# Kernel optimization log

Measured on AMD Instinct MI355X. Metric: run time of the kernel, lower is better.

## Reference

```python
import jax, jax.numpy as jnp
import numpy as np

B, T, D = 2, 2048, 2048
NH, NKV = 16, 4
HD = D // NH  # 128
BASE, TSL = 10000.0, 1024


def rotary_tables(T, hd, base=BASE, tsl=TSL):
    # Matches Rotary.forward with rd == hd (rd=0 in __init__ -> full head dim).
    ar = jnp.arange(0, hd, 2, dtype=jnp.float32) / hd
    if T <= tsl:
        inv = 1.0 / (base ** ar)
    else:
        # NTK-style rescale; note right-assoc exponent in original torch code:
        # 1/(base * (T/tsl) ** ((rd/(rd-2)) ** ar))
        inv = 1.0 / (base * jnp.power(T / tsl, jnp.power(hd / (hd - 2.0), ar)))
    f = jnp.outer(jnp.arange(T, dtype=jnp.float32), inv)  # [T, hd//2]
    cos = jnp.cos(f)[None, :, None, :]  # [1,T,1,hd//2]
    sin = jnp.sin(f)[None, :, None, :]
    return cos, sin


def apply_rope(x, cos, sin):
    # full-dim rope: split halves, rotate
    h = x.shape[-1] // 2
    x1, x2 = x[..., :h], x[..., h:]
    return jnp.concatenate((x1 * cos + x2 * sin, -x1 * sin + x2 * cos), axis=-1)


def rms_norm(x):
    eps = jnp.finfo(x.dtype).eps
    return x * jax.lax.rsqrt(jnp.mean(x * x, axis=-1, keepdims=True) + eps)


def setup_inputs() -> dict:
    key = jax.random.key(0)
    k0, k1, k2, k3, k4 = jax.random.split(key, 5)
    s = 0.02
    return {
        "x": jax.random.normal(k0, (B, T, D), jnp.float32),
        "qw": jax.random.normal(k1, (NH * HD, D), jnp.float32) * s,
        "kw": jax.random.normal(k2, (NKV * HD, D), jnp.float32) * s,
        "vw": jax.random.normal(k3, (NKV * HD, D), jnp.float32) * s,
        "ow": jax.random.normal(k4, (D, D), jnp.float32) * s,
        "qg": jnp.ones((NH,), jnp.float32),
    }


def reference(x, qw, kw, vw, ow, qg):
    Bx, Tx, Dx = x.shape
    q = (x @ qw.T).reshape(Bx, Tx, NH, HD)
    k = (x @ kw.T).reshape(Bx, Tx, NKV, HD)
    v = (x @ vw.T).reshape(Bx, Tx, NKV, HD)
    q = rms_norm(q)
    k = rms_norm(k)
    cos, sin = rotary_tables(Tx, HD)
    q = apply_rope(q, cos, sin) * qg[None, None, :, None]
    k = apply_rope(k, cos, sin)
    # GQA: repeat kv heads
    r = NH // NKV
    k = jnp.repeat(k, r, axis=2)  # [B,T,NH,HD]
    v = jnp.repeat(v, r, axis=2)
    scale = 1.0 / jnp.sqrt(jnp.asarray(HD, q.dtype))
    scores = jnp.einsum("bqhd,bkhd->bhqk", q, k) * scale  # [B,NH,T,T]
    causal = jnp.tril(jnp.ones((Tx, Tx), dtype=bool))
    scores = jnp.where(causal[None, None, :, :], scores, jnp.asarray(-jnp.inf, scores.dtype))
    attn = jax.nn.softmax(scores, axis=-1)
    y = jnp.einsum("bhqk,bkhd->bqhd", attn, v)  # [B,T,NH,HD]
    return y.reshape(Bx, Tx, Dx) @ ow.T
```

## Files before the change

### kernel.cpp

```cpp
#include <hip/hip_runtime.h>
#include <hip/hip_bf16.h>
#include <stdint.h>


typedef __attribute__((ext_vector_type(8))) short short8;
typedef __attribute__((ext_vector_type(4))) float f32x4;
typedef __attribute__((ext_vector_type(16))) float f32x16;

#define GLOAD16(gp, lp) \
  __builtin_amdgcn_global_load_lds((const __attribute__((address_space(1))) void*)(gp), \
                                   (__attribute__((address_space(3))) void*)(lp), 16, 0, 0)

#define BAR() do { asm volatile("" ::: "memory"); __builtin_amdgcn_s_barrier(); asm volatile("" ::: "memory"); } while (0)

__device__ __forceinline__ float bf2f(unsigned short u) {
  union { unsigned int i; float f; } v; v.i = ((unsigned int)u) << 16; return v.f;
}
__device__ __forceinline__ unsigned short f2bf(float f) {
  union { float fl; unsigned int i; } v; v.fl = f;
  unsigned int r = v.i + 0x7fffu + ((v.i >> 16) & 1u);
  return (unsigned short)(r >> 16);
}
__device__ __forceinline__ unsigned pk2(float a, float b) {
  return (unsigned)f2bf(a) | ((unsigned)f2bf(b) << 16);
// ... 151 lines not shown
#pragma unroll
      for (int ks = 0; ks < 2; ++ks) af[iq][ks] = *(const short8*)(Ab + oA[iq][ks]);
#pragma unroll
    for (int jj = 0; jj < JQ; ++jj)
#pragma unroll
      for (int ks = 0; ks < 2; ++ks) b0[jj][ks] = *(const short8*)(Bb + oB[jj][ks]);
    MM(0, 0, b0);
    BAR();
    if (s + 2 < NS) STA((s + 2) << 6, 0, dq);
#pragma unroll
    for (int jj = 0; jj < JQ; ++jj)
#pragma unroll
      for (int ks = 0; ks < 2; ++ks) b1[jj][ks] = *(const short8*)(Bb + BSZ + oB[jj][ks]);
    MM(0, 1, b1);
    BAR();
    if (s + 2 < NS) STB((s + 2) << 6, 0, dq);
#pragma unroll
    for (int iq = 0; iq < IQ; ++iq)
#pragma unroll
      for (int ks = 0; ks < 2; ++ks) af[iq][ks] = *(const short8*)(Ab + ASZ + oA[iq][ks]);
    MM(1, 0, b0);
    BAR();
    if (s + 2 < NS) STB((s + 2) << 6, 1, dq);
    MM(1, 1, b1);
    if (s + 2 < NS) VMC(); else VM0();
    BAR();
  }
#undef VMC
#undef VM0
#undef MM

#pragma unroll
  for (int ih = 0; ih < 2; ++ih)
#pragma unroll
    for (int iq = 0; iq < IQ; ++iq) {
      int row = m0 + wr * 2 * S + ih * S + iq * 16 + lane_g * 4;
#pragma unroll
      for (int jh = 0; jh < 2; ++jh)
#pragma unroll
        for (int jj = 0; jj < JQ; ++jj) {
          int col = n0 + wc * (NB / 4) + jh * (NB / 8) + jj * 16 + lane_r;
#pragma unroll
          for (int r = 0; r < 4; ++r) {
            float v = acc[ih * IQ + iq][jh * JQ + jj][r];
            if (OUTF)
              ((float*)Cp)[(size_t)(row + r) * N + col] = v;
            else
              ((unsigned short*)Cp)[(size_t)(row + r) * N + col] = f2bf(v);
          }
        }
    }
}

__global__ __launch_bounds__(256) void normrope_kernel(unsigned short* __restrict__ qkv,
                                                       const float* __restrict__ cost,
                                                       const float* __restrict__ sint,
                                                       const float* __restrict__ qg) {
  const int tid = threadIdx.x, l = tid & 63, w = tid >> 6;
  int row = blockIdx.x * 4 + w;
  int tok = row / 20, hh = row - tok * 20;
  int t = tok & 2047;
  bool isq = hh < 16;
  int col0 = isq ? hh * 128 : 2048 + (hh - 16) * 128;
  unsigned short* p = qkv + (size_t)tok * 3072 + col0 + 2 * l;
  unsigned int u = *(const unsigned int*)p;
  float x0 = bf2f((unsigned short)(u & 0xffffu));
  float x1 = bf2f((unsigned short)(u >> 16));
  float ss = x0 * x0 + x1 * x1;
#pragma unroll
  for (int m = 1; m < 64; m <<= 1) ss += __shfl_xor(ss, m);
  float rn = rsqrtf(ss * (1.0f / 128.0f) + 1.1920928955078125e-07f);
  float n0 = x0 * rn, n1 = x1 * rn;
  float p0 = __shfl_xor(n0, 32);
  float p1 = __shfl_xor(n1, 32);
  int jj = (2 * l) & 63;
  float c0 = cost[t * 64 + jj], c1 = cost[t * 64 + jj + 1];
  float s0 = sint[t * 64 + jj], s1 = sint[t * 64 + jj + 1];
  float o0, o1;
  if (l < 32) { o0 = n0 * c0 + p0 * s0; o1 = n1 * c1 + p1 * s1; }
  else        { o0 = -p0 * s0 + n0 * c0; o1 = -p1 * s1 + n1 * c1; }
  if (isq) { float g = qg[hh] * 0.08838834764831845f * 1.4426950408889634f; o0 *= g; o1 *= g; }
  *(unsigned int*)p = pk2(o0, o1);
}

__global__ __launch_bounds__(256) void vtrans_kernel(const unsigned short* __restrict__ qkv,
                                                     unsigned short* __restrict__ vtg) {
  __shared__ unsigned short tile[64][132];
  int bid = blockIdx.x;
  int pan = bid & 7, tt = bid >> 3;
  int b = pan >> 2, kvh = pan & 3;
  int t0 = tt * 64;
  const unsigned short* src = qkv + ((size_t)(b * 2048 + t0)) * 3072 + 2560 + kvh * 128;
#pragma unroll
  for (int i = 0; i < 8; ++i) {
    int idx = i * 256 + threadIdx.x;
    int row = idx >> 5, c4 = idx & 31;
    uint2 v = *(const uint2*)(src + (size_t)row * 3072 + c4 * 4);
    *(uint2*)&tile[row][c4 * 4] = v;
  }
  __syncthreads();
  unsigned short* dst = vtg + (size_t)pan * 262144 + t0;
#pragma unroll
  for (int i = 0; i < 8; ++i) {
    int idx = i * 256 + threadIdx.x;
    int d = idx >> 4, tc = idx & 15;
    unsigned short a0 = tile[tc * 4 + 0][d], a1 = tile[tc * 4 + 1][d];
    unsigned short a2 = tile[tc * 4 + 2][d], a3 = tile[tc * 4 + 3][d];
    uint2 o; o.x = (unsigned)a0 | ((unsigned)a1 << 16);
    o.y = (unsigned)a2 | ((unsigned)a3 << 16);
    *(uint2*)(dst + (size_t)d * 2048 + tc * 4) = o;
  }
}

__global__ __launch_bounds__(512) void attn_fa7(const unsigned short* __restrict__ qkv,
                                                const unsigned short* __restrict__ vtg,
                                                unsigned short* __restrict__ y) {
  extern __shared__ char smc[];
  const int tid = threadIdx.x;
  const int l = tid & 63, w = tid >> 6;
  const int lq = l & 31, hi = l >> 5;
  const int g = w & 3, hh = w >> 2;

  int n = blockIdx.x;
  int pan = n & 7;
  int b = pan >> 2, kvh = pan & 3;
  int idx2 = n >> 3;
  int h = kvh * 4 + (idx2 & 3);
  int pairIdx = idx2 >> 2;
  const size_t rowbase = (size_t)b * 2048;
  const unsigned short* kvK = qkv + rowbase * 3072;
  const unsigned short* vtp = vtg + (size_t)pan * 262144;

  int kg[2], vg[2], sl[2];
#pragma unroll
  for (int t = 0; t < 2; ++t) {
    int idx = t * 512 + tid;
    { int row = idx >> 4, c = idx & 15, gc = c ^ (row & 7);
      kg[t] = row * 3072 + 2048 + kvh * 128 + gc * 8; }
    { int d = idx >> 3, c = idx & 7, gc = c ^ (d & 7);
      vg[t] = d * 2048 + gc * 8; }
    sl[t] = idx * 16;
  }
  const int swq = (lq & 7) << 4;
  const int krow = (hh * 32 + lq) * 256;
  int oxk[8];
#pragma unroll
  for (int ds = 0; ds < 8; ++ds) oxk[ds] = (ds * 32 + hi * 16) ^ swq;
  const int vrow = lq * 128;
  int oxv[2];
#pragma unroll
  for (int ksl = 0; ksl < 2; ++ksl) oxv[ksl] = (hh * 64 + ksl * 32 + hi * 16) ^ swq;
  const int mab = (g * 64 + l) * 256;
  const int mlb = 65536 + (g * 64 + l) * 8;
  const int lsw = (l & 7) << 4;

  auto STAGE = [&](int tile, int bufsel) {
    const unsigned short* srcK = kvK + (size_t)tile * 64 * 3072;
    const unsigned short* srcV = vtp + tile * 64;
    char* kd = smc + bufsel * 16384;
    char* vd = smc + 32768 + bufsel * 16384;
#pragma unroll
    for (int t = 0; t < 2; ++t) {
      GLOAD16(srcK + kg[t], kd + sl[t]);
      GLOAD16(srcV + vg[t], vd + sl[t]);
    }
  };

#pragma unroll 1
  for (int phase = 0; phase < 2; ++phase) {
    const int qt = phase ? pairIdx : 15 - pairIdx;
    const int q0 = qt * 128;
    const int nkb = 2 * qt + 2;
    const int wrow0 = q0 + g * 32;
    const int qrow = wrow0 + lq;

    STAGE(0, 0);
    short8 qf[8];
#pragma unroll
    for (int ds = 0; ds < 8; ++ds)
      qf[ds] = *(const short8*)(qkv + (rowbase + qrow) * 3072 + h * 128 + ds * 16 + hi * 8);

    f32x16 acc[4];
#pragma unroll
    for (int dt = 0; dt < 4; ++dt)
#pragma unroll
      for (int jj = 0; jj < 16; ++jj) acc[dt][jj] = 0.f;
    float mrun = -1e30f, lrun = 0.f;

    __syncthreads();

#pragma unroll 1
    for (int kb = 0; kb < nkb; ++kb) {
      const int cur = kb & 1;
      if (kb + 1 < nkb) STAGE(kb + 1, cur ^ 1);
      const int j0 = kb * 64;
      if (j0 + hh * 32 <= wrow0) {
        const int kbb = cur * 16384;
        const int vbb = 32768 + cur * 16384;
        f32x16 s;
#pragma unroll
        for (int jj = 0; jj < 16; ++jj) s[jj] = 0.f;
        __builtin_amdgcn_s_setprio(1);
#pragma unroll
        for (int ds = 0; ds < 8; ++ds) {
          short8 kf = *(const short8*)(smc + kbb + krow + oxk[ds]);
          s = __builtin_amdgcn_mfma_f32_32x32x16_bf16(kf, qf[ds], s, 0, 0, 0);
        }
        __builtin_amdgcn_s_setprio(0);
        const int rq = qrow - j0 - hh * 32;
        if (rq < 31) {
#pragma unroll
          for (int jj = 0; jj < 16; ++jj) {
            int kl = (jj & 3) + 8 * (jj >> 2) + 4 * hi;
            s[jj] = (kl > rq) ? -1e30f : s[jj];
          }
        }
        float pmax = s[0];
#pragma unroll
        for (int jj = 1; jj < 16; ++jj) pmax = fmaxf(pmax, s[jj]);
        pmax = fmaxf(pmax, __shfl_xor(pmax, 32));
        if (!__all(pmax - mrun <= 11.5f)) {
          float mn = fmaxf(mrun, pmax);
          float corr = exp2f(mrun - mn);
          lrun *= corr;
#pragma unroll
          for (int dt = 0; dt < 4; ++dt)
#pragma unroll
            for (int jj = 0; jj < 16; ++jj) acc[dt][jj] *= corr;
          mrun = mn;
        }
        float rs = 0.f;
#pragma unroll
        for (int jj = 0; jj < 16; ++jj) { s[jj] = exp2f(s[jj] - mrun); rs += s[jj]; }
        rs += __shfl_xor(rs, 32);
        lrun += rs;
        unsigned r[8];
#pragma unroll
        for (int j = 0; j < 4; ++j) {
          asm("v_cvt_pk_bf16_f32 %0, %1, %2" : "=v"(r[2 * j]) : "v"(s[4 * j]), "v"(s[4 * j + 1]));
          asm("v_cvt_pk_bf16_f32 %0, %1, %2" : "=v"(r[2 * j + 1]) : "v"(s[4 * j + 2]), "v"(s[4 * j + 3]));
        }
        __builtin_amdgcn_s_setprio(1);
#pragma unroll
        for (int ksl = 0; ksl < 2; ++ksl) {
          unsigned w0 = r[4 * ksl], w2 = r[4 * ksl + 2];
          asm("v_permlane32_swap_b32 %0, %1" : "+v"(w0), "+v"(w2));
          unsigned w1 = r[4 * ksl + 1], w3 = r[4 * ksl + 3];
          asm("v_permlane32_swap_b32 %0, %1" : "+v"(w1), "+v"(w3));
          union { unsigned u[4]; short8 s8; } pu;
          pu.u[0] = w0; pu.u[1] = w1; pu.u[2] = w2; pu.u[3] = w3;
          short8 pf = pu.s8;
#pragma unroll
          for (int dt = 0; dt < 4; ++dt) {
            short8 vf = *(const short8*)(smc + vbb + dt * 4096 + vrow + oxv[ksl]);
            acc[dt] = __builtin_amdgcn_mfma_f32_32x32x16_bf16(vf, pf, acc[dt], 0, 0, 0);
          }
        }
        __builtin_amdgcn_s_setprio(0);
      }
      __syncthreads();
    }
    if (hh) {
#pragma unroll
      for (int dt = 0; dt < 4; ++dt)
#pragma unroll
        for (int q4 = 0; q4 < 4; ++q4) {
          f32x4 v = {acc[dt][4 * q4], acc[dt][4 * q4 + 1], acc[dt][4 * q4 + 2], acc[dt][4 * q4 + 3]};
          *(f32x4*)(smc + mab + ((dt * 64 + q4 * 16) ^ lsw)) = v;
        }
      *(float2*)(smc + mlb) = {mrun, lrun};
    }
    __syncthreads();
    if (!hh) {
      float2 ml = *(const float2*)(smc + mlb);
      float mx = fmaxf(mrun, ml.x);
      float sc0 = exp2f(mrun - mx), sc1 = exp2f(ml.x - mx);
      lrun = lrun * sc0 + ml.y * sc1;
#pragma unroll
      for (int dt = 0; dt < 4; ++dt)
#pragma unroll
        for (int q4 = 0; q4 < 4; ++q4) {
          f32x4 v = *(const f32x4*)(smc + mab + ((dt * 64 + q4 * 16) ^ lsw));
#pragma unroll
          for (int r = 0; r < 4; ++r)
            acc[dt][4 * q4 + r] = acc[dt][4 * q4 + r] * sc0 + v[r] * sc1;
        }
    }
    __syncthreads();
    if (!hh) {
      float linv = 1.0f / lrun;
      unsigned short* yrow = y + (rowbase + qrow) * 2048 + h * 128;
#pragma unroll
      for (int dt = 0; dt < 4; ++dt)
#pragma unroll
        for (int m = 0; m < 4; ++m) {
          uint2 o;
          o.x = pk2(acc[dt][4 * m] * linv, acc[dt][4 * m + 1] * linv);
          o.y = pk2(acc[dt][4 * m + 2] * linv, acc[dt][4 * m + 3] * linv);
          *(uint2*)(yrow + dt * 32 + m * 8 + hi * 4) = o;
        }
    }
  }
}

extern "C" void kernel_launch(void* const* d_in, const int* in_sizes, int n_in,
                              void* d_out, int out_size, void* d_ws, size_t ws_size,
                              hipStream_t stream) {
  (void)in_sizes; (void)n_in; (void)out_size; (void)ws_size;
  const float* x  = (const float*)d_in[0];
  const float* qw = (const float*)d_in[1];
  const float* kw = (const float*)d_in[2];
  const float* vw = (const float*)d_in[3];
  const float* ow = (const float*)d_in[4];
  const float* qg = (const float*)d_in[5];

  char* ws = (char*)d_ws;
  unsigned short* xb   = (unsigned short*)(ws + 0);
  unsigned short* vtg  = (unsigned short*)(ws + 0);
  unsigned short* wqkv = (unsigned short*)(ws + 16777216);
  unsigned short* owb  = (unsigned short*)(ws + 29360128);
  unsigned short* qkvb = (unsigned short*)(ws + 37748736);
  unsigned short* y    = (unsigned short*)(ws + 62914560);
  float* cost          = (float*)(ws + 79691776);
  float* sint          = (float*)(ws + 80216064);

  prep_kernel<<<18944, 256, 0, stream>>>(x, qw, kw, vw, ow, xb, wqkv, owb, cost, sint);
  gemm8ph<4, 384, 0><<<256, 512, 131072, stream>>>(xb, wqkv, qkvb, 32, 8, 3072, 2048);
  normrope_kernel<<<20480, 256, 0, stream>>>(qkvb, cost, sint, qg);
  vtrans_kernel<<<256, 256, 0, stream>>>(qkvb, vtg);
  attn_fa7<<<256, 512, 67584, stream>>>(qkvb, vtg, y);
  gemm8ph<4, 256, 1><<<256, 512, 98304, stream>>>(y, owb, d_out, 32, 8, 2048, 2048);
}
```

Baseline: 189.2 us.

## Triple-buffer K/V in attention with QK^T lookahead and merge normrope with V transpose

The attention kernel moves from double to triple buffering of K/V tiles in LDS and prefetches two tiles ahead. It also computes the QK^T scores for the next tile before running softmax and PV on the current tile, so MFMA work can overlap with exp and reduction work. Separately, the norm/rope kernel and the V-transpose kernel become one launch with block-index dispatch, removing one kernel launch. The costs are more LDS per block (about 100KB), more registers for the extra score tile, and a possible race, since the V-transpose blocks read V columns that the norm/rope blocks in the same launch do not write.

```diff
diff --git a/kernel.cpp b/kernel.cpp
--- a/kernel.cpp
+++ b/kernel.cpp
@@ -227,67 +227,69 @@
     }
 }
 
-__global__ __launch_bounds__(256) void normrope_kernel(unsigned short* __restrict__ qkv,
-                                                       const float* __restrict__ cost,
-                                                       const float* __restrict__ sint,
-                                                       const float* __restrict__ qg) {
-  const int tid = threadIdx.x, l = tid & 63, w = tid >> 6;
-  int row = blockIdx.x * 4 + w;
-  int tok = row / 20, hh = row - tok * 20;
-  int t = tok & 2047;
-  bool isq = hh < 16;
-  int col0 = isq ? hh * 128 : 2048 + (hh - 16) * 128;
-  unsigned short* p = qkv + (size_t)tok * 3072 + col0 + 2 * l;
-  unsigned int u = *(const unsigned int*)p;
-  float x0 = bf2f((unsigned short)(u & 0xffffu));
-  float x1 = bf2f((unsigned short)(u >> 16));
-  float ss = x0 * x0 + x1 * x1;
-#pragma unroll
-  for (int m = 1; m < 64; m <<= 1) ss += __shfl_xor(ss, m);
-  float rn = rsqrtf(ss * (1.0f / 128.0f) + 1.1920928955078125e-07f);
-  float n0 = x0 * rn, n1 = x1 * rn;
-  float p0 = __shfl_xor(n0, 32);
-  float p1 = __shfl_xor(n1, 32);
-  int jj = (2 * l) & 63;
-  float c0 = cost[t * 64 + jj], c1 = cost[t * 64 + jj + 1];
-  float s0 = sint[t * 64 + jj], s1 = sint[t * 64 + jj + 1];
-  float o0, o1;
-  if (l < 32) { o0 = n0 * c0 + p0 * s0; o1 = n1 * c1 + p1 * s1; }
-  else        { o0 = -p0 * s0 + n0 * c0; o1 = -p1 * s1 + n1 * c1; }
-  if (isq) { float g = qg[hh] * 0.08838834764831845f * 1.4426950408889634f; o0 *= g; o1 *= g; }
-  *(unsigned int*)p = pk2(o0, o1);
-}
-
-__global__ __launch_bounds__(256) void vtrans_kernel(const unsigned short* __restrict__ qkv,
-                                                     unsigned short* __restrict__ vtg) {
+__global__ __launch_bounds__(256) void normrope_vt_kernel(unsigned short* __restrict__ qkv,
+                                                          const float* __restrict__ cost,
+                                                          const float* __restrict__ sint,
+                                                          const float* __restrict__ qg,
+                                                          unsigned short* __restrict__ vtg) {
   __shared__ unsigned short tile[64][132];
   int bid = blockIdx.x;
-  int pan = bid & 7, tt = bid >> 3;
-  int b = pan >> 2, kvh = pan & 3;
-  int t0 = tt * 64;
-  const unsigned short* src = qkv + ((size_t)(b * 2048 + t0)) * 3072 + 2560 + kvh * 128;
-#pragma unroll
-  for (int i = 0; i < 8; ++i) {
-    int idx = i * 256 + threadIdx.x;
-    int row = idx >> 5, c4 = idx & 31;
-    uint2 v = *(const uint2*)(src + (size_t)row * 3072 + c4 * 4);
-    *(uint2*)&tile[row][c4 * 4] = v;
-  }
-  __syncthreads();
-  unsigned short* dst = vtg + (size_t)pan * 262144 + t0;
-#pragma unroll
-  for (int i = 0; i < 8; ++i) {
-    int idx = i * 256 + threadIdx.x;
-    int d = idx >> 4, tc = idx & 15;
-    unsigned short a0 = tile[tc * 4 + 0][d], a1 = tile[tc * 4 + 1][d];
-    unsigned short a2 = tile[tc * 4 + 2][d], a3 = tile[tc * 4 + 3][d];
-    uint2 o; o.x = (unsigned)a0 | ((unsigned)a1 << 16);
-    o.y = (unsigned)a2 | ((unsigned)a3 << 16);
-    *(uint2*)(dst + (size_t)d * 2048 + tc * 4) = o;
-  }
-}
-
-__global__ __launch_bounds__(512) void attn_fa7(const unsigned short* __restrict__ qkv,
+  const int tid = threadIdx.x;
+  if (bid < 20480) {
+    const int l = tid & 63, w = tid >> 6;
+    int row = bid * 4 + w;
+    int tok = row / 20, hh = row - tok * 20;
+    int t = tok & 2047;
+    bool isq = hh < 16;
+    int col0 = isq ? hh * 128 : 2048 + (hh - 16) * 128;
+    unsigned short* p = qkv + (size_t)tok * 3072 + col0 + 2 * l;
+    unsigned int u = *(const unsigned int*)p;
+    float x0 = bf2f((unsigned short)(u & 0xffffu));
+    float x1 = bf2f((unsigned short)(u >> 16));
+    float ss = x0 * x0 + x1 * x1;
+#pragma unroll
+    for (int m = 1; m < 64; m <<= 1) ss += __shfl_xor(ss, m);
+    float rn = rsqrtf(ss * (1.0f / 128.0f) + 1.1920928955078125e-07f);
+    float n0 = x0 * rn, n1 = x1 * rn;
+    float p0 = __shfl_xor(n0, 32);
+    float p1 = __shfl_xor(n1, 32);
+    int jj = (2 * l) & 63;
+    float c0 = cost[t * 64 + jj], c1 = cost[t * 64 + jj + 1];
+    float s0 = sint[t * 64 + jj], s1 = sint[t * 64 + jj + 1];
+    float o0, o1;
+    if (l < 32) { o0 = n0 * c0 + p0 * s0; o1 = n1 * c1 + p1 * s1; }
+    else        { o0 = -p0 * s0 + n0 * c0; o1 = -p1 * s1 + n1 * c1; }
+    if (isq) { float g = qg[hh] * 0.08838834764831845f * 1.4426950408889634f; o0 *= g; o1 *= g; }
+    *(unsigned int*)p = pk2(o0, o1);
+  } else {
+    int bid2 = bid - 20480;
+    int pan = bid2 & 7, tt = bid2 >> 3;
+    int b = pan >> 2, kvh = pan & 3;
+    int t0 = tt * 64;
+    const unsigned short* src = qkv + ((size_t)(b * 2048 + t0)) * 3072 + 2560 + kvh * 128;
+#pragma unroll
+    for (int i = 0; i < 8; ++i) {
+      int idx = i * 256 + tid;
+      int row = idx >> 5, c4 = idx & 31;
+      uint2 v = *(const uint2*)(src + (size_t)row * 3072 + c4 * 4);
+      *(uint2*)&tile[row][c4 * 4] = v;
+    }
+    __syncthreads();
+    unsigned short* dst = vtg + (size_t)pan * 262144 + t0;
+#pragma unroll
+    for (int i = 0; i < 8; ++i) {
+      int idx = i * 256 + tid;
+      int d = idx >> 4, tc = idx & 15;
+      unsigned short a0 = tile[tc * 4 + 0][d], a1 = tile[tc * 4 + 1][d];
+      unsigned short a2 = tile[tc * 4 + 2][d], a3 = tile[tc * 4 + 3][d];
+      uint2 o; o.x = (unsigned)a0 | ((unsigned)a1 << 16);
+      o.y = (unsigned)a2 | ((unsigned)a3 << 16);
+      *(uint2*)(dst + (size_t)d * 2048 + tc * 4) = o;
+    }
+  }
+}
+
+__global__ __launch_bounds__(512) void attn_fa9(const unsigned short* __restrict__ qkv,
                                                 const unsigned short* __restrict__ vtg,
                                                 unsigned short* __restrict__ y) {
   extern __shared__ char smc[];
@@ -326,14 +328,14 @@
 #pragma unroll
   for (int ksl = 0; ksl < 2; ++ksl) oxv[ksl] = (hh * 64 + ksl * 32 + hi * 16) ^ swq;
   const int mab = (g * 64 + l) * 256;
-  const int mlb = 65536 + (g * 64 + l) * 8;
+  const int mlb = 98304 + (g * 64 + l) * 8;
   const int lsw = (l & 7) << 4;
 
-  auto STAGE = [&](int tile, int bufsel) {
+  auto STAGE = [&](int tile, int slot) {
     const unsigned short* srcK = kvK + (size_t)tile * 64 * 3072;
     const unsigned short* srcV = vtp + tile * 64;
-    char* kd = smc + bufsel * 16384;
-    char* vd = smc + 32768 + bufsel * 16384;
+    char* kd = smc + slot * 16384;
+    char* vd = smc + 49152 + slot * 16384;
 #pragma unroll
     for (int t = 0; t < 2; ++t) {
       GLOAD16(srcK + kg[t], kd + sl[t]);
@@ -350,6 +352,7 @@
     const int qrow = wrow0 + lq;
 
     STAGE(0, 0);
+    STAGE(1, 1);
     short8 qf[8];
 #pragma unroll
     for (int ds = 0; ds < 8; ++ds)
@@ -362,37 +365,48 @@
       for (int jj = 0; jj < 16; ++jj) acc[dt][jj] = 0.f;
     float mrun = -1e30f, lrun = 0.f;
 
+    auto QKC = [&](int kb, int slot) -> f32x16 {
+      const int kbb = slot * 16384;
+      f32x16 s;
+#pragma unroll
+      for (int jj = 0; jj < 16; ++jj) s[jj] = 0.f;
+#pragma unroll
+      for (int ds = 0; ds < 8; ++ds) {
+        short8 kf = *(const short8*)(smc + kbb + krow + oxk[ds]);
+        s = __builtin_amdgcn_mfma_f32_32x32x16_bf16(kf, qf[ds], s, 0, 0, 0);
+      }
+      const int rq = qrow - kb * 64 - hh * 32;
+      if (rq < 31) {
+#pragma unroll
+        for (int jj = 0; jj < 16; ++jj) {
+          int kl = (jj & 3) + 8 * (jj >> 2) + 4 * hi;
+          s[jj] = (kl > rq) ? -1e30f : s[jj];
+        }
+      }
+      return s;
+    };
+
     __syncthreads();
+
+    f32x16 scur;
+    bool act0 = (hh * 32 <= wrow0);
+    if (act0) scur = QKC(0, 0);
 
 #pragma unroll 1
     for (int kb = 0; kb < nkb; ++kb) {
-      const int cur = kb & 1;
-      if (kb + 1 < nkb) STAGE(kb + 1, cur ^ 1);
-      const int j0 = kb * 64;
-      if (j0 + hh * 32 <= wrow0) {
-        const int kbb = cur * 16384;
-        const int vbb = 32768 + cur * 16384;
-        f32x16 s;
-#pragma unroll
-        for (int jj = 0; jj < 16; ++jj) s[jj] = 0.f;
+      if (kb + 2 < nkb) STAGE(kb + 2, (kb + 2) % 3);
+      const bool actn = (kb + 1 < nkb) && ((kb + 1) * 64 + hh * 32 <= wrow0);
+      const bool act = (kb * 64 + hh * 32 <= wrow0);
+      f32x16 snx;
+      if (actn) {
         __builtin_amdgcn_s_setprio(1);
-#pragma unroll
-        for (int ds = 0; ds < 8; ++ds) {
-          short8 kf = *(const short8*)(smc + kbb + krow + oxk[ds]);
-          s = __builtin_amdgcn_mfma_f32_32x32x16_bf16(kf, qf[ds], s, 0, 0, 0);
-        }
+        snx = QKC(kb + 1, (kb + 1) % 3);
         __builtin_amdgcn_s_setprio(0);
-        const int rq = qrow - j0 - hh * 32;
-        if (rq < 31) {
-#pragma unroll
-          for (int jj = 0; jj < 16; ++jj) {
-            int kl = (jj & 3) + 8 * (jj >> 2) + 4 * hi;
-            s[jj] = (kl > rq) ? -1e30f : s[jj];
-          }
-        }
-        float pmax = s[0];
-#pragma unroll
-        for (int jj = 1; jj < 16; ++jj) pmax = fmaxf(pmax, s[jj]);
+      }
+      if (act) {
+        float pmax = scur[0];
+#pragma unroll
+        for (int jj = 1; jj < 16; ++jj) pmax = fmaxf(pmax, scur[jj]);
         pmax = fmaxf(pmax, __shfl_xor(pmax, 32));
         if (!__all(pmax - mrun <= 11.5f)) {
           float mn = fmaxf(mrun, pmax);
@@ -406,15 +420,16 @@
         }
         float rs = 0.f;
 #pragma unroll
-        for (int jj = 0; jj < 16; ++jj) { s[jj] = exp2f(s[jj] - mrun); rs += s[jj]; }
+        for (int jj = 0; jj < 16; ++jj) { scur[jj] = exp2f(scur[jj] - mrun); rs += scur[jj]; }
         rs += __shfl_xor(rs, 32);
         lrun += rs;
         unsigned r[8];
 #pragma unroll
         for (int j = 0; j < 4; ++j) {
-          asm("v_cvt_pk_bf16_f32 %0, %1, %2" : "=v"(r[2 * j]) : "v"(s[4 * j]), "v"(s[4 * j + 1]));
-          asm("v_cvt_pk_bf16_f32 %0, %1, %2" : "=v"(r[2 * j + 1]) : "v"(s[4 * j + 2]), "v"(s[4 * j + 3]));
-        }
+          asm("v_cvt_pk_bf16_f32 %0, %1, %2" : "=v"(r[2 * j]) : "v"(scur[4 * j]), "v"(scur[4 * j + 1]));
+          asm("v_cvt_pk_bf16_f32 %0, %1, %2" : "=v"(r[2 * j + 1]) : "v"(scur[4 * j + 2]), "v"(scur[4 * j + 3]));
+        }
+        const int vbb = 49152 + (kb % 3) * 16384;
         __builtin_amdgcn_s_setprio(1);
 #pragma unroll
         for (int ksl = 0; ksl < 2; ++ksl) {
@@ -433,6 +448,7 @@
         }
         __builtin_amdgcn_s_setprio(0);
       }
+      scur = snx;
       __syncthreads();
     }
     if (hh) {
@@ -501,8 +517,7 @@
 
   prep_kernel<<<18944, 256, 0, stream>>>(x, qw, kw, vw, ow, xb, wqkv, owb, cost, sint);
   gemm8ph<4, 384, 0><<<256, 512, 131072, stream>>>(xb, wqkv, qkvb, 32, 8, 3072, 2048);
-  normrope_kernel<<<20480, 256, 0, stream>>>(qkvb, cost, sint, qg);
-  vtrans_kernel<<<256, 256, 0, stream>>>(qkvb, vtg);
-  attn_fa7<<<256, 512, 67584, stream>>>(qkvb, vtg, y);
+  normrope_vt_kernel<<<20736, 256, 0, stream>>>(qkvb, cost, sint, qg, vtg);
+  attn_fa9<<<256, 512, 100352, stream>>>(qkvb, vtg, y);
   gemm8ph<4, 256, 1><<<256, 512, 98304, stream>>>(y, owb, d_out, 32, 8, 2048, 2048);
 }
```

After: 189.9 us. Within noise of the previous version (+0.4%).

## Merge norm-rope and V-transpose kernels; shrink attention blocks to 64-row tiles

Applied to the files above, without the earlier changes.

Merges the norm+rope kernel and the V-transpose kernel into one launch by assigning a block range to each, removing a launch boundary. The attention kernel now uses 256-thread blocks covering 64 query rows instead of 512 threads covering 128, with twice as many blocks. It also uses a single-buffered K/V stage (load, barrier, compute) instead of double buffering, halving LDS so about four blocks can fit per CU. The trade-off is that prefetch overlap is lost in exchange for higher occupancy and finer causal load balancing, and the merged kernel no longer guarantees the V-transpose runs after norm-rope, though the two touch disjoint columns.

```diff
diff --git a/kernel.cpp b/kernel.cpp
--- a/kernel.cpp
+++ b/kernel.cpp
@@ -227,74 +227,76 @@
     }
 }
 
-__global__ __launch_bounds__(256) void normrope_kernel(unsigned short* __restrict__ qkv,
-                                                       const float* __restrict__ cost,
-                                                       const float* __restrict__ sint,
-                                                       const float* __restrict__ qg) {
-  const int tid = threadIdx.x, l = tid & 63, w = tid >> 6;
-  int row = blockIdx.x * 4 + w;
-  int tok = row / 20, hh = row - tok * 20;
-  int t = tok & 2047;
-  bool isq = hh < 16;
-  int col0 = isq ? hh * 128 : 2048 + (hh - 16) * 128;
-  unsigned short* p = qkv + (size_t)tok * 3072 + col0 + 2 * l;
-  unsigned int u = *(const unsigned int*)p;
-  float x0 = bf2f((unsigned short)(u & 0xffffu));
-  float x1 = bf2f((unsigned short)(u >> 16));
-  float ss = x0 * x0 + x1 * x1;
-#pragma unroll
-  for (int m = 1; m < 64; m <<= 1) ss += __shfl_xor(ss, m);
-  float rn = rsqrtf(ss * (1.0f / 128.0f) + 1.1920928955078125e-07f);
-  float n0 = x0 * rn, n1 = x1 * rn;
-  float p0 = __shfl_xor(n0, 32);
-  float p1 = __shfl_xor(n1, 32);
-  int jj = (2 * l) & 63;
-  float c0 = cost[t * 64 + jj], c1 = cost[t * 64 + jj + 1];
-  float s0 = sint[t * 64 + jj], s1 = sint[t * 64 + jj + 1];
-  float o0, o1;
-  if (l < 32) { o0 = n0 * c0 + p0 * s0; o1 = n1 * c1 + p1 * s1; }
-  else        { o0 = -p0 * s0 + n0 * c0; o1 = -p1 * s1 + n1 * c1; }
-  if (isq) { float g = qg[hh] * 0.08838834764831845f * 1.4426950408889634f; o0 *= g; o1 *= g; }
-  *(unsigned int*)p = pk2(o0, o1);
-}
-
-__global__ __launch_bounds__(256) void vtrans_kernel(const unsigned short* __restrict__ qkv,
-                                                     unsigned short* __restrict__ vtg) {
+__global__ __launch_bounds__(256) void normrope_vt_kernel(unsigned short* __restrict__ qkv,
+                                                          const float* __restrict__ cost,
+                                                          const float* __restrict__ sint,
+                                                          const float* __restrict__ qg,
+                                                          unsigned short* __restrict__ vtg) {
   __shared__ unsigned short tile[64][132];
   int bid = blockIdx.x;
-  int pan = bid & 7, tt = bid >> 3;
-  int b = pan >> 2, kvh = pan & 3;
-  int t0 = tt * 64;
-  const unsigned short* src = qkv + ((size_t)(b * 2048 + t0)) * 3072 + 2560 + kvh * 128;
-#pragma unroll
-  for (int i = 0; i < 8; ++i) {
-    int idx = i * 256 + threadIdx.x;
-    int row = idx >> 5, c4 = idx & 31;
-    uint2 v = *(const uint2*)(src + (size_t)row * 3072 + c4 * 4);
-    *(uint2*)&tile[row][c4 * 4] = v;
-  }
-  __syncthreads();
-  unsigned short* dst = vtg + (size_t)pan * 262144 + t0;
-#pragma unroll
-  for (int i = 0; i < 8; ++i) {
-    int idx = i * 256 + threadIdx.x;
-    int d = idx >> 4, tc = idx & 15;
-    unsigned short a0 = tile[tc * 4 + 0][d], a1 = tile[tc * 4 + 1][d];
-    unsigned short a2 = tile[tc * 4 + 2][d], a3 = tile[tc * 4 + 3][d];
-    uint2 o; o.x = (unsigned)a0 | ((unsigned)a1 << 16);
-    o.y = (unsigned)a2 | ((unsigned)a3 << 16);
-    *(uint2*)(dst + (size_t)d * 2048 + tc * 4) = o;
-  }
-}
-
-__global__ __launch_bounds__(512) void attn_fa7(const unsigned short* __restrict__ qkv,
-                                                const unsigned short* __restrict__ vtg,
-                                                unsigned short* __restrict__ y) {
+  const int tid = threadIdx.x;
+  if (bid < 20480) {
+    const int l = tid & 63, w = tid >> 6;
+    int row = bid * 4 + w;
+    int tok = row / 20, hh = row - tok * 20;
+    int t = tok & 2047;
+    bool isq = hh < 16;
+    int col0 = isq ? hh * 128 : 2048 + (hh - 16) * 128;
+    unsigned short* p = qkv + (size_t)tok * 3072 + col0 + 2 * l;
+    unsigned int u = *(const unsigned int*)p;
+    float x0 = bf2f((unsigned short)(u & 0xffffu));
+    float x1 = bf2f((unsigned short)(u >> 16));
+    float ss = x0 * x0 + x1 * x1;
+#pragma unroll
+    for (int m = 1; m < 64; m <<= 1) ss += __shfl_xor(ss, m);
+    float rn = rsqrtf(ss * (1.0f / 128.0f) + 1.1920928955078125e-07f);
+    float n0 = x0 * rn, n1 = x1 * rn;
+    float p0 = __shfl_xor(n0, 32);
+    float p1 = __shfl_xor(n1, 32);
+    int jj = (2 * l) & 63;
+    float c0 = cost[t * 64 + jj], c1 = cost[t * 64 + jj + 1];
+    float s0 = sint[t * 64 + jj], s1 = sint[t * 64 + jj + 1];
+    float o0, o1;
+    if (l < 32) { o0 = n0 * c0 + p0 * s0; o1 = n1 * c1 + p1 * s1; }
+    else        { o0 = -p0 * s0 + n0 * c0; o1 = -p1 * s1 + n1 * c1; }
+    if (isq) { float g = qg[hh] * 0.08838834764831845f * 1.4426950408889634f; o0 *= g; o1 *= g; }
+    *(unsigned int*)p = pk2(o0, o1);
+  } else {
+    int bid2 = bid - 20480;
+    int pan = bid2 & 7, tt = bid2 >> 3;
+    int b = pan >> 2, kvh = pan & 3;
+    int t0 = tt * 64;
+    const unsigned short* src = qkv + ((size_t)(b * 2048 + t0)) * 3072 + 2560 + kvh * 128;
+#pragma unroll
+    for (int i = 0; i < 8; ++i) {
+      int idx = i * 256 + tid;
+      int row = idx >> 5, c4 = idx & 31;
+      uint2 v = *(const uint2*)(src + (size_t)row * 3072 + c4 * 4);
+      *(uint2*)&tile[row][c4 * 4] = v;
+    }
+    __syncthreads();
+    unsigned short* dst = vtg + (size_t)pan * 262144 + t0;
+#pragma unroll
+    for (int i = 0; i < 8; ++i) {
+      int idx = i * 256 + tid;
+      int d = idx >> 4, tc = idx & 15;
+      unsigned short a0 = tile[tc * 4 + 0][d], a1 = tile[tc * 4 + 1][d];
+      unsigned short a2 = tile[tc * 4 + 2][d], a3 = tile[tc * 4 + 3][d];
+      uint2 o; o.x = (unsigned)a0 | ((unsigned)a1 << 16);
+      o.y = (unsigned)a2 | ((unsigned)a3 << 16);
+      *(uint2*)(dst + (size_t)d * 2048 + tc * 4) = o;
+    }
+  }
+}
+
+__global__ __launch_bounds__(256, 4) void attn_fa12(const unsigned short* __restrict__ qkv,
+                                                    const unsigned short* __restrict__ vtg,
+                                                    unsigned short* __restrict__ y) {
   extern __shared__ char smc[];
   const int tid = threadIdx.x;
   const int l = tid & 63, w = tid >> 6;
   const int lq = l & 31, hi = l >> 5;
-  const int g = w & 3, hh = w >> 2;
+  const int g = w & 1, hh = w >> 1;
 
   int n = blockIdx.x;
   int pan = n & 7;
@@ -306,16 +308,11 @@
   const unsigned short* kvK = qkv + rowbase * 3072;
   const unsigned short* vtp = vtg + (size_t)pan * 262144;
 
-  int kg[2], vg[2], sl[2];
-#pragma unroll
-  for (int t = 0; t < 2; ++t) {
-    int idx = t * 512 + tid;
-    { int row = idx >> 4, c = idx & 15, gc = c ^ (row & 7);
-      kg[t] = row * 3072 + 2048 + kvh * 128 + gc * 8; }
-    { int d = idx >> 3, c = idx & 7, gc = c ^ (d & 7);
-      vg[t] = d * 2048 + gc * 8; }
-    sl[t] = idx * 16;
-  }
+  const int kbase = (tid >> 4) * 3072 + 2048 + kvh * 128 + ((tid & 15) ^ ((tid >> 4) & 7)) * 8;
+  const int vbase = (tid >> 3) * 2048 + ((tid & 7) ^ ((tid >> 3) & 7)) * 8;
+  const int slK = tid * 16;
+  const int slV = 16384 + tid * 16;
+
   const int swq = (lq & 7) << 4;
   const int krow = (hh * 32 + lq) * 256;
   int oxk[8];
@@ -325,31 +322,28 @@
   int oxv[2];
 #pragma unroll
   for (int ksl = 0; ksl < 2; ++ksl) oxv[ksl] = (hh * 64 + ksl * 32 + hi * 16) ^ swq;
-  const int mab = (g * 64 + l) * 256;
-  const int mlb = 65536 + (g * 64 + l) * 8;
+  const int mslot = (g * 64 + l) * 256;
+  const int mlb = 32768 + (g * 64 + l) * 8;
   const int lsw = (l & 7) << 4;
 
-  auto STAGE = [&](int tile, int bufsel) {
+  auto STAGE = [&](int tile) {
     const unsigned short* srcK = kvK + (size_t)tile * 64 * 3072;
     const unsigned short* srcV = vtp + tile * 64;
-    char* kd = smc + bufsel * 16384;
-    char* vd = smc + 32768 + bufsel * 16384;
-#pragma unroll
-    for (int t = 0; t < 2; ++t) {
-      GLOAD16(srcK + kg[t], kd + sl[t]);
-      GLOAD16(srcV + vg[t], vd + sl[t]);
+#pragma unroll
+    for (int t = 0; t < 4; ++t) {
+      GLOAD16(srcK + kbase + t * 49152, smc + slK + t * 4096);
+      GLOAD16(srcV + vbase + t * 65536, smc + slV + t * 4096);
     }
   };
 
 #pragma unroll 1
   for (int phase = 0; phase < 2; ++phase) {
-    const int qt = phase ? pairIdx : 15 - pairIdx;
-    const int q0 = qt * 128;
-    const int nkb = 2 * qt + 2;
+    const int ht = phase ? pairIdx : 31 - pairIdx;
+    const int q0 = ht * 64;
+    const int nkb = ht + 1;
     const int wrow0 = q0 + g * 32;
     const int qrow = wrow0 + lq;
 
-    STAGE(0, 0);
     short8 qf[8];
 #pragma unroll
     for (int ds = 0; ds < 8; ++ds)
@@ -362,23 +356,19 @@
       for (int jj = 0; jj < 16; ++jj) acc[dt][jj] = 0.f;
     float mrun = -1e30f, lrun = 0.f;
 
-    __syncthreads();
-
 #pragma unroll 1
     for (int kb = 0; kb < nkb; ++kb) {
-      const int cur = kb & 1;
-      if (kb + 1 < nkb) STAGE(kb + 1, cur ^ 1);
+      STAGE(kb);
+      __syncthreads();
       const int j0 = kb * 64;
       if (j0 + hh * 32 <= wrow0) {
-        const int kbb = cur * 16384;
-        const int vbb = 32768 + cur * 16384;
         f32x16 s;
 #pragma unroll
         for (int jj = 0; jj < 16; ++jj) s[jj] = 0.f;
         __builtin_amdgcn_s_setprio(1);
 #pragma unroll
         for (int ds = 0; ds < 8; ++ds) {
-          short8 kf = *(const short8*)(smc + kbb + krow + oxk[ds]);
+          short8 kf = *(const short8*)(smc + krow + oxk[ds]);
           s = __builtin_amdgcn_mfma_f32_32x32x16_bf16(kf, qf[ds], s, 0, 0, 0);
         }
         __builtin_amdgcn_s_setprio(0);
@@ -427,7 +417,7 @@
           short8 pf = pu.s8;
 #pragma unroll
           for (int dt = 0; dt < 4; ++dt) {
-            short8 vf = *(const short8*)(smc + vbb + dt * 4096 + vrow + oxv[ksl]);
+            short8 vf = *(const short8*)(smc + 16384 + dt * 4096 + vrow + oxv[ksl]);
             acc[dt] = __builtin_amdgcn_mfma_f32_32x32x16_bf16(vf, pf, acc[dt], 0, 0, 0);
           }
         }
@@ -441,7 +431,7 @@
 #pragma unroll
         for (int q4 = 0; q4 < 4; ++q4) {
           f32x4 v = {acc[dt][4 * q4], acc[dt][4 * q4 + 1], acc[dt][4 * q4 + 2], acc[dt][4 * q4 + 3]};
-          *(f32x4*)(smc + mab + ((dt * 64 + q4 * 16) ^ lsw)) = v;
+          *(f32x4*)(smc + mslot + ((dt * 64 + q4 * 16) ^ lsw)) = v;
         }
       *(float2*)(smc + mlb) = {mrun, lrun};
     }
@@ -455,14 +445,11 @@
       for (int dt = 0; dt < 4; ++dt)
 #pragma unroll
         for (int q4 = 0; q4 < 4; ++q4) {
-          f32x4 v = *(const f32x4*)(smc + mab + ((dt * 64 + q4 * 16) ^ lsw));
-#pragma unroll
-          for (int r = 0; r < 4; ++r)
-            acc[dt][4 * q4 + r] = acc[dt][4 * q4 + r] * sc0 + v[r] * sc1;
-        }
-    }
-    __syncthreads();
-    if (!hh) {
+          f32x4 v = *(const f32x4*)(smc + mslot + ((dt * 64 + q4 * 16) ^ lsw));
+#pragma unroll
+          for (int r2 = 0; r2 < 4; ++r2)
+            acc[dt][4 * q4 + r2] = acc[dt][4 * q4 + r2] * sc0 + v[r2] * sc1;
+        }
       float linv = 1.0f / lrun;
       unsigned short* yrow = y + (rowbase + qrow) * 2048 + h * 128;
 #pragma unroll
@@ -475,6 +462,7 @@
           *(uint2*)(yrow + dt * 32 + m * 8 + hi * 4) = o;
         }
     }
+    __syncthreads();
   }
 }
 
@@ -501,8 +489,7 @@
 
   prep_kernel<<<18944, 256, 0, stream>>>(x, qw, kw, vw, ow, xb, wqkv, owb, cost, sint);
   gemm8ph<4, 384, 0><<<256, 512, 131072, stream>>>(xb, wqkv, qkvb, 32, 8, 3072, 2048);
-  normrope_kernel<<<20480, 256, 0, stream>>>(qkvb, cost, sint, qg);
-  vtrans_kernel<<<256, 256, 0, stream>>>(qkvb, vtg);
-  attn_fa7<<<256, 512, 67584, stream>>>(qkvb, vtg, y);
+  normrope_vt_kernel<<<20736, 256, 0, stream>>>(qkvb, cost, sint, qg, vtg);
+  attn_fa12<<<512, 256, 33792, stream>>>(qkvb, vtg, y);
   gemm8ph<4, 256, 1><<<256, 512, 98304, stream>>>(y, owb, d_out, 32, 8, 2048, 2048);
 }
```

After: 233.4 us. 1.23x slower.

## Merge normrope and V-transpose launches; split attention phases into separate blocks

Applied to the files above, without the earlier changes.

Combines the norm+RoPE kernel and the V transpose kernel into one launch, with block ranges dispatching to either path. This removes one launch and lets the two run concurrently, which is safe because they touch disjoint columns (normrope touches only Q/K, vtrans reads only V). The attention kernel no longer loops over two causal q-tile phases per block; it launches 512 blocks, each handling one q-tile. That doubles the grid for better CU occupancy and load balance, at the cost of losing the paired long/short work balancing inside a block and repeating some per-block setup.

```diff
diff --git a/kernel.cpp b/kernel.cpp
--- a/kernel.cpp
+++ b/kernel.cpp
@@ -227,69 +227,71 @@
     }
 }
 
-__global__ __launch_bounds__(256) void normrope_kernel(unsigned short* __restrict__ qkv,
-                                                       const float* __restrict__ cost,
-                                                       const float* __restrict__ sint,
-                                                       const float* __restrict__ qg) {
-  const int tid = threadIdx.x, l = tid & 63, w = tid >> 6;
-  int row = blockIdx.x * 4 + w;
-  int tok = row / 20, hh = row - tok * 20;
-  int t = tok & 2047;
-  bool isq = hh < 16;
-  int col0 = isq ? hh * 128 : 2048 + (hh - 16) * 128;
-  unsigned short* p = qkv + (size_t)tok * 3072 + col0 + 2 * l;
-  unsigned int u = *(const unsigned int*)p;
-  float x0 = bf2f((unsigned short)(u & 0xffffu));
-  float x1 = bf2f((unsigned short)(u >> 16));
-  float ss = x0 * x0 + x1 * x1;
-#pragma unroll
-  for (int m = 1; m < 64; m <<= 1) ss += __shfl_xor(ss, m);
-  float rn = rsqrtf(ss * (1.0f / 128.0f) + 1.1920928955078125e-07f);
-  float n0 = x0 * rn, n1 = x1 * rn;
-  float p0 = __shfl_xor(n0, 32);
-  float p1 = __shfl_xor(n1, 32);
-  int jj = (2 * l) & 63;
-  float c0 = cost[t * 64 + jj], c1 = cost[t * 64 + jj + 1];
-  float s0 = sint[t * 64 + jj], s1 = sint[t * 64 + jj + 1];
-  float o0, o1;
-  if (l < 32) { o0 = n0 * c0 + p0 * s0; o1 = n1 * c1 + p1 * s1; }
-  else        { o0 = -p0 * s0 + n0 * c0; o1 = -p1 * s1 + n1 * c1; }
-  if (isq) { float g = qg[hh] * 0.08838834764831845f * 1.4426950408889634f; o0 *= g; o1 *= g; }
-  *(unsigned int*)p = pk2(o0, o1);
-}
-
-__global__ __launch_bounds__(256) void vtrans_kernel(const unsigned short* __restrict__ qkv,
-                                                     unsigned short* __restrict__ vtg) {
+__global__ __launch_bounds__(256) void normrope_vt_kernel(unsigned short* __restrict__ qkv,
+                                                          const float* __restrict__ cost,
+                                                          const float* __restrict__ sint,
+                                                          const float* __restrict__ qg,
+                                                          unsigned short* __restrict__ vtg) {
   __shared__ unsigned short tile[64][132];
   int bid = blockIdx.x;
-  int pan = bid & 7, tt = bid >> 3;
-  int b = pan >> 2, kvh = pan & 3;
-  int t0 = tt * 64;
-  const unsigned short* src = qkv + ((size_t)(b * 2048 + t0)) * 3072 + 2560 + kvh * 128;
-#pragma unroll
-  for (int i = 0; i < 8; ++i) {
-    int idx = i * 256 + threadIdx.x;
-    int row = idx >> 5, c4 = idx & 31;
-    uint2 v = *(const uint2*)(src + (size_t)row * 3072 + c4 * 4);
-    *(uint2*)&tile[row][c4 * 4] = v;
-  }
-  __syncthreads();
-  unsigned short* dst = vtg + (size_t)pan * 262144 + t0;
-#pragma unroll
-  for (int i = 0; i < 8; ++i) {
-    int idx = i * 256 + threadIdx.x;
-    int d = idx >> 4, tc = idx & 15;
-    unsigned short a0 = tile[tc * 4 + 0][d], a1 = tile[tc * 4 + 1][d];
-    unsigned short a2 = tile[tc * 4 + 2][d], a3 = tile[tc * 4 + 3][d];
-    uint2 o; o.x = (unsigned)a0 | ((unsigned)a1 << 16);
-    o.y = (unsigned)a2 | ((unsigned)a3 << 16);
-    *(uint2*)(dst + (size_t)d * 2048 + tc * 4) = o;
-  }
-}
-
-__global__ __launch_bounds__(512) void attn_fa7(const unsigned short* __restrict__ qkv,
-                                                const unsigned short* __restrict__ vtg,
-                                                unsigned short* __restrict__ y) {
+  const int tid = threadIdx.x;
+  if (bid < 20480) {
+    const int l = tid & 63, w = tid >> 6;
+    int row = bid * 4 + w;
+    int tok = row / 20, hh = row - tok * 20;
+    int t = tok & 2047;
+    bool isq = hh < 16;
+    int col0 = isq ? hh * 128 : 2048 + (hh - 16) * 128;
+    unsigned short* p = qkv + (size_t)tok * 3072 + col0 + 2 * l;
+    unsigned int u = *(const unsigned int*)p;
+    float x0 = bf2f((unsigned short)(u & 0xffffu));
+    float x1 = bf2f((unsigned short)(u >> 16));
+    float ss = x0 * x0 + x1 * x1;
+#pragma unroll
+    for (int m = 1; m < 64; m <<= 1) ss += __shfl_xor(ss, m);
+    float rn = rsqrtf(ss * (1.0f / 128.0f) + 1.1920928955078125e-07f);
+    float n0 = x0 * rn, n1 = x1 * rn;
+    float p0 = __shfl_xor(n0, 32);
+    float p1 = __shfl_xor(n1, 32);
+    int jj = (2 * l) & 63;
+    float c0 = cost[t * 64 + jj], c1 = cost[t * 64 + jj + 1];
+    float s0 = sint[t * 64 + jj], s1 = sint[t * 64 + jj + 1];
+    float o0, o1;
+    if (l < 32) { o0 = n0 * c0 + p0 * s0; o1 = n1 * c1 + p1 * s1; }
+    else        { o0 = -p0 * s0 + n0 * c0; o1 = -p1 * s1 + n1 * c1; }
+    if (isq) { float g = qg[hh] * 0.08838834764831845f * 1.4426950408889634f; o0 *= g; o1 *= g; }
+    *(unsigned int*)p = pk2(o0, o1);
+  } else {
+    int bid2 = bid - 20480;
+    int pan = bid2 & 7, tt = bid2 >> 3;
+    int b = pan >> 2, kvh = pan & 3;
+    int t0 = tt * 64;
+    const unsigned short* src = qkv + ((size_t)(b * 2048 + t0)) * 3072 + 2560 + kvh * 128;
+#pragma unroll
+    for (int i = 0; i < 8; ++i) {
+      int idx = i * 256 + tid;
+      int row = idx >> 5, c4 = idx & 31;
+      uint2 v = *(const uint2*)(src + (size_t)row * 3072 + c4 * 4);
+      *(uint2*)&tile[row][c4 * 4] = v;
+    }
+    __syncthreads();
+    unsigned short* dst = vtg + (size_t)pan * 262144 + t0;
+#pragma unroll
+    for (int i = 0; i < 8; ++i) {
+      int idx = i * 256 + tid;
+      int d = idx >> 4, tc = idx & 15;
+      unsigned short a0 = tile[tc * 4 + 0][d], a1 = tile[tc * 4 + 1][d];
+      unsigned short a2 = tile[tc * 4 + 2][d], a3 = tile[tc * 4 + 3][d];
+      uint2 o; o.x = (unsigned)a0 | ((unsigned)a1 << 16);
+      o.y = (unsigned)a2 | ((unsigned)a3 << 16);
+      *(uint2*)(dst + (size_t)d * 2048 + tc * 4) = o;
+    }
+  }
+}
+
+__global__ __launch_bounds__(512) void attn_fa13(const unsigned short* __restrict__ qkv,
+                                                 const unsigned short* __restrict__ vtg,
+                                                 unsigned short* __restrict__ y) {
   extern __shared__ char smc[];
   const int tid = threadIdx.x;
   const int l = tid & 63, w = tid >> 6;
@@ -297,11 +299,13 @@
   const int g = w & 3, hh = w >> 2;
 
   int n = blockIdx.x;
-  int pan = n & 7;
+  int n8 = n & 255;
+  int pan = n8 & 7;
   int b = pan >> 2, kvh = pan & 3;
-  int idx2 = n >> 3;
+  int idx2 = n8 >> 3;
   int h = kvh * 4 + (idx2 & 3);
   int pairIdx = idx2 >> 2;
+  const int qt = (n >= 256) ? pairIdx : 15 - pairIdx;
   const size_t rowbase = (size_t)b * 2048;
   const unsigned short* kvK = qkv + rowbase * 3072;
   const unsigned short* vtp = vtg + (size_t)pan * 262144;
@@ -341,140 +345,133 @@
     }
   };
 
+  const int q0 = qt * 128;
+  const int nkb = 2 * qt + 2;
+  const int wrow0 = q0 + g * 32;
+  const int qrow = wrow0 + lq;
+
+  STAGE(0, 0);
+  short8 qf[8];
+#pragma unroll
+  for (int ds = 0; ds < 8; ++ds)
+    qf[ds] = *(const short8*)(qkv + (rowbase + qrow) * 3072 + h * 128 + ds * 16 + hi * 8);
+
+  f32x16 acc[4];
+#pragma unroll
+  for (int dt = 0; dt < 4; ++dt)
+#pragma unroll
+    for (int jj = 0; jj < 16; ++jj) acc[dt][jj] = 0.f;
+  float mrun = -1e30f, lrun = 0.f;
+
+  __syncthreads();
+
 #pragma unroll 1
-  for (int phase = 0; phase < 2; ++phase) {
-    const int qt = phase ? pairIdx : 15 - pairIdx;
-    const int q0 = qt * 128;
-    const int nkb = 2 * qt + 2;
-    const int wrow0 = q0 + g * 32;
-    const int qrow = wrow0 + lq;
-
-    STAGE(0, 0);
-    short8 qf[8];
-#pragma unroll
-    for (int ds = 0; ds < 8; ++ds)
-      qf[ds] = *(const short8*)(qkv + (rowbase + qrow) * 3072 + h * 128 + ds * 16 + hi * 8);
-
-    f32x16 acc[4];
+  for (int kb = 0; kb < nkb; ++kb) {
+    const int cur = kb & 1;
+    if (kb + 1 < nkb) STAGE(kb + 1, cur ^ 1);
+    const int j0 = kb * 64;
+    if (j0 + hh * 32 <= wrow0) {
+      const int kbb = cur * 16384;
+      const int vbb = 32768 + cur * 16384;
+      f32x16 s;
+#pragma unroll
+      for (int jj = 0; jj < 16; ++jj) s[jj] = 0.f;
+      __builtin_amdgcn_s_setprio(1);
+#pragma unroll
+      for (int ds = 0; ds < 8; ++ds) {
+        short8 kf = *(const short8*)(smc + kbb + krow + oxk[ds]);
+        s = __builtin_amdgcn_mfma_f32_32x32x16_bf16(kf, qf[ds], s, 0, 0, 0);
+      }
+      __builtin_amdgcn_s_setprio(0);
+      const int rq = qrow - j0 - hh * 32;
+      if (rq < 31) {
+#pragma unroll
+        for (int jj = 0; jj < 16; ++jj) {
+          int kl = (jj & 3) + 8 * (jj >> 2) + 4 * hi;
+          s[jj] = (kl > rq) ? -1e30f : s[jj];
+        }
+      }
+      float pmax = s[0];
+#pragma unroll
+      for (int jj = 1; jj < 16; ++jj) pmax = fmaxf(pmax, s[jj]);
+      pmax = fmaxf(pmax, __shfl_xor(pmax, 32));
+      if (!__all(pmax - mrun <= 11.5f)) {
+        float mn = fmaxf(mrun, pmax);
+        float corr = exp2f(mrun - mn);
+        lrun *= corr;
+#pragma unroll
+        for (int dt = 0; dt < 4; ++dt)
+#pragma unroll
+          for (int jj = 0; jj < 16; ++jj) acc[dt][jj] *= corr;
+        mrun = mn;
+      }
+      float rs = 0.f;
+#pragma unroll
+      for (int jj = 0; jj < 16; ++jj) { s[jj] = exp2f(s[jj] - mrun); rs += s[jj]; }
+      rs += __shfl_xor(rs, 32);
+      lrun += rs;
+      unsigned r[8];
+#pragma unroll
+      for (int j = 0; j < 4; ++j) {
+        asm("v_cvt_pk_bf16_f32 %0, %1, %2" : "=v"(r[2 * j]) : "v"(s[4 * j]), "v"(s[4 * j + 1]));
+        asm("v_cvt_pk_bf16_f32 %0, %1, %2" : "=v"(r[2 * j + 1]) : "v"(s[4 * j + 2]), "v"(s[4 * j + 3]));
+      }
+      __builtin_amdgcn_s_setprio(1);
+#pragma unroll
+      for (int ksl = 0; ksl < 2; ++ksl) {
+        unsigned w0 = r[4 * ksl], w2 = r[4 * ksl + 2];
+        asm("v_permlane32_swap_b32 %0, %1" : "+v"(w0), "+v"(w2));
+        unsigned w1 = r[4 * ksl + 1], w3 = r[4 * ksl + 3];
+        asm("v_permlane32_swap_b32 %0, %1" : "+v"(w1), "+v"(w3));
+        union { unsigned u[4]; short8 s8; } pu;
+        pu.u[0] = w0; pu.u[1] = w1; pu.u[2] = w2; pu.u[3] = w3;
+        short8 pf = pu.s8;
+#pragma unroll
+        for (int dt = 0; dt < 4; ++dt) {
+          short8 vf = *(const short8*)(smc + vbb + dt * 4096 + vrow + oxv[ksl]);
+          acc[dt] = __builtin_amdgcn_mfma_f32_32x32x16_bf16(vf, pf, acc[dt], 0, 0, 0);
+        }
+      }
+      __builtin_amdgcn_s_setprio(0);
+    }
+    __syncthreads();
+  }
+  if (hh) {
 #pragma unroll
     for (int dt = 0; dt < 4; ++dt)
 #pragma unroll
-      for (int jj = 0; jj < 16; ++jj) acc[dt][jj] = 0.f;
-    float mrun = -1e30f, lrun = 0.f;
-
-    __syncthreads();
-
-#pragma unroll 1
-    for (int kb = 0; kb < nkb; ++kb) {
-      const int cur = kb & 1;
-      if (kb + 1 < nkb) STAGE(kb + 1, cur ^ 1);
-      const int j0 = kb * 64;
-      if (j0 + hh * 32 <= wrow0) {
-        const int kbb = cur * 16384;
-        const int vbb = 32768 + cur * 16384;
-        f32x16 s;
-#pragma unroll
-        for (int jj = 0; jj < 16; ++jj) s[jj] = 0.f;
-        __builtin_amdgcn_s_setprio(1);
-#pragma unroll
-        for (int ds = 0; ds < 8; ++ds) {
-          short8 kf = *(const short8*)(smc + kbb + krow + oxk[ds]);
-          s = __builtin_amdgcn_mfma_f32_32x32x16_bf16(kf, qf[ds], s, 0, 0, 0);
-        }
-        __builtin_amdgcn_s_setprio(0);
-        const int rq = qrow - j0 - hh * 32;
-        if (rq < 31) {
-#pragma unroll
-          for (int jj = 0; jj < 16; ++jj) {
-            int kl = (jj & 3) + 8 * (jj >> 2) + 4 * hi;
-            s[jj] = (kl > rq) ? -1e30f : s[jj];
-          }
-        }
-        float pmax = s[0];
-#pragma unroll
-        for (int jj = 1; jj < 16; ++jj) pmax = fmaxf(pmax, s[jj]);
-        pmax = fmaxf(pmax, __shfl_xor(pmax, 32));
-        if (!__all(pmax - mrun <= 11.5f)) {
-          float mn = fmaxf(mrun, pmax);
-          float corr = exp2f(mrun - mn);
-          lrun *= corr;
-#pragma unroll
-          for (int dt = 0; dt < 4; ++dt)
-#pragma unroll
-            for (int jj = 0; jj < 16; ++jj) acc[dt][jj] *= corr;
-          mrun = mn;
-        }
-        float rs = 0.f;
-#pragma unroll
-        for (int jj = 0; jj < 16; ++jj) { s[jj] = exp2f(s[jj] - mrun); rs += s[jj]; }
-        rs += __shfl_xor(rs, 32);
-        lrun += rs;
-        unsigned r[8];
-#pragma unroll
-        for (int j = 0; j < 4; ++j) {
-          asm("v_cvt_pk_bf16_f32 %0, %1, %2" : "=v"(r[2 * j]) : "v"(s[4 * j]), "v"(s[4 * j + 1]));
-          asm("v_cvt_pk_bf16_f32 %0, %1, %2" : "=v"(r[2 * j + 1]) : "v"(s[4 * j + 2]), "v"(s[4 * j + 3]));
-        }
-        __builtin_amdgcn_s_setprio(1);
-#pragma unroll
-        for (int ksl = 0; ksl < 2; ++ksl) {
-          unsigned w0 = r[4 * ksl], w2 = r[4 * ksl + 2];
-          asm("v_permlane32_swap_b32 %0, %1" : "+v"(w0), "+v"(w2));
-          unsigned w1 = r[4 * ksl + 1], w3 = r[4 * ksl + 3];
-          asm("v_permlane32_swap_b32 %0, %1" : "+v"(w1), "+v"(w3));
-          union { unsigned u[4]; short8 s8; } pu;
-          pu.u[0] = w0; pu.u[1] = w1; pu.u[2] = w2; pu.u[3] = w3;
-          short8 pf = pu.s8;
-#pragma unroll
-          for (int dt = 0; dt < 4; ++dt) {
-            short8 vf = *(const short8*)(smc + vbb + dt * 4096 + vrow + oxv[ksl]);
-            acc[dt] = __builtin_amdgcn_mfma_f32_32x32x16_bf16(vf, pf, acc[dt], 0, 0, 0);
-          }
-        }
-        __builtin_amdgcn_s_setprio(0);
-      }
-      __syncthreads();
-    }
-    if (hh) {
-#pragma unroll
-      for (int dt = 0; dt < 4; ++dt)
-#pragma unroll
-        for (int q4 = 0; q4 < 4; ++q4) {
-          f32x4 v = {acc[dt][4 * q4], acc[dt][4 * q4 + 1], acc[dt][4 * q4 + 2], acc[dt][4 * q4 + 3]};
-          *(f32x4*)(smc + mab + ((dt * 64 + q4 * 16) ^ lsw)) = v;
-        }
-      *(float2*)(smc + mlb) = {mrun, lrun};
-    }
-    __syncthreads();
-    if (!hh) {
-      float2 ml = *(const float2*)(smc + mlb);
-      float mx = fmaxf(mrun, ml.x);
-      float sc0 = exp2f(mrun - mx), sc1 = exp2f(ml.x - mx);
-      lrun = lrun * sc0 + ml.y * sc1;
-#pragma unroll
-      for (int dt = 0; dt < 4; ++dt)
-#pragma unroll
-        for (int q4 = 0; q4 < 4; ++q4) {
-          f32x4 v = *(const f32x4*)(smc + mab + ((dt * 64 + q4 * 16) ^ lsw));
-#pragma unroll
-          for (int r = 0; r < 4; ++r)
-            acc[dt][4 * q4 + r] = acc[dt][4 * q4 + r] * sc0 + v[r] * sc1;
-        }
-    }
-    __syncthreads();
-    if (!hh) {
-      float linv = 1.0f / lrun;
-      unsigned short* yrow = y + (rowbase + qrow) * 2048 + h * 128;
-#pragma unroll
-      for (int dt = 0; dt < 4; ++dt)
-#pragma unroll
-        for (int m = 0; m < 4; ++m) {
-          uint2 o;
-          o.x = pk2(acc[dt][4 * m] * linv, acc[dt][4 * m + 1] * linv);
-          o.y = pk2(acc[dt][4 * m + 2] * linv, acc[dt][4 * m + 3] * linv);
-          *(uint2*)(yrow + dt * 32 + m * 8 + hi * 4) = o;
-        }
-    }
+      for (int q4 = 0; q4 < 4; ++q4) {
+        f32x4 v = {acc[dt][4 * q4], acc[dt][4 * q4 + 1], acc[dt][4 * q4 + 2], acc[dt][4 * q4 + 3]};
+        *(f32x4*)(smc + mab + ((dt * 64 + q4 * 16) ^ lsw)) = v;
+      }
+    *(float2*)(smc + mlb) = {mrun, lrun};
+  }
+  __syncthreads();
+  if (!hh) {
+    float2 ml = *(const float2*)(smc + mlb);
+    float mx = fmaxf(mrun, ml.x);
+    float sc0 = exp2f(mrun - mx), sc1 = exp2f(ml.x - mx);
+    lrun = lrun * sc0 + ml.y * sc1;
+#pragma unroll
+    for (int dt = 0; dt < 4; ++dt)
+#pragma unroll
+      for (int q4 = 0; q4 < 4; ++q4) {
+        f32x4 v = *(const f32x4*)(smc + mab + ((dt * 64 + q4 * 16) ^ lsw));
+#pragma unroll
+        for (int r2 = 0; r2 < 4; ++r2)
+          acc[dt][4 * q4 + r2] = acc[dt][4 * q4 + r2] * sc0 + v[r2] * sc1;
+      }
+    float linv = 1.0f / lrun;
+    unsigned short* yrow = y + (rowbase + qrow) * 2048 + h * 128;
+#pragma unroll
+    for (int dt = 0; dt < 4; ++dt)
+#pragma unroll
+      for (int m = 0; m < 4; ++m) {
+        uint2 o;
+        o.x = pk2(acc[dt][4 * m] * linv, acc[dt][4 * m + 1] * linv);
+        o.y = pk2(acc[dt][4 * m + 2] * linv, acc[dt][4 * m + 3] * linv);
+        *(uint2*)(yrow + dt * 32 + m * 8 + hi * 4) = o;
+      }
   }
 }
 
@@ -501,8 +498,7 @@
 
   prep_kernel<<<18944, 256, 0, stream>>>(x, qw, kw, vw, ow, xb, wqkv, owb, cost, sint);
   gemm8ph<4, 384, 0><<<256, 512, 131072, stream>>>(xb, wqkv, qkvb, 32, 8, 3072, 2048);
-  normrope_kernel<<<20480, 256, 0, stream>>>(qkvb, cost, sint, qg);
-  vtrans_kernel<<<256, 256, 0, stream>>>(qkvb, vtg);
-  attn_fa7<<<256, 512, 67584, stream>>>(qkvb, vtg, y);
+  normrope_vt_kernel<<<20736, 256, 0, stream>>>(qkvb, cost, sint, qg, vtg);
+  attn_fa13<<<512, 512, 67584, stream>>>(qkvb, vtg, y);
   gemm8ph<4, 256, 1><<<256, 512, 98304, stream>>>(y, owb, d_out, 32, 8, 2048, 2048);
 }
```

Result: slower. 200.9 us (+6.2%).
